# Kernel tuning notes

Measured on AMD Instinct MI355X. Metric: run time of the kernel, lower is better.

Reference implementation:

```python
import jax, jax.numpy as jnp
import numpy as np

N_NODES = 40000
N_EDGES = 640000
IN_F = 128
HID = 128
MAX_ITERS = 8  # torch loop runs MAX_ITERS + 1 state updates (epsilon=None)


def setup_inputs() -> dict:
    key = jax.random.key(0)
    k1, k2, k3, k4, k5, k6 = jax.random.split(key, 6)
    x = jax.random.normal(k1, (N_NODES, IN_F), dtype=jnp.float32)
    edge_index = jax.random.randint(k2, (2, N_EDGES), 0, N_NODES, dtype=jnp.int64)
    scale = 0.1 / np.sqrt(HID)  # keep tanh out of deep saturation (ESN-style spectral scaling)
    w_in0 = jax.random.normal(k3, (HID, IN_F), dtype=jnp.float32) * scale   # layer 0 input_weight
    w_rec0 = jax.random.normal(k4, (HID, HID), dtype=jnp.float32) * scale   # layer 0 recurrent_weight
    w_in1 = jax.random.normal(k5, (HID, HID), dtype=jnp.float32) * scale    # layer 1 input_weight
    w_rec1 = jax.random.normal(k6, (HID, HID), dtype=jnp.float32) * scale   # layer 1 recurrent_weight
    return {"edge_index": edge_index, "x": x,
            "w_in0": w_in0, "w_rec0": w_rec0, "w_in1": w_in1, "w_rec1": w_rec1}


def _embed(x_proj, w_rec, src, dst):
    # Fixed-point iteration: state = tanh(x_proj + aggr(state) @ w_rec)
    # aggr = sum of source-node states scattered to destination nodes (PyG aggr='add').
    state0 = jnp.zeros_like(x_proj)

    def step(state, _):
        aggr = jax.ops.segment_sum(state[src], dst, num_segments=N_NODES)  # [N, H]
        new_state = jnp.tanh(x_proj + aggr @ w_rec)
        return new_state, None

    state, _ = jax.lax.scan(step, state0, None, length=MAX_ITERS + 1)
    return state


def reference(edge_index, x, w_in0, w_rec0, w_in1, w_rec1):
    src, dst = edge_index[0], edge_index[1]
    h0 = _embed(x @ w_in0.T, w_rec0, src, dst)    # layer 0 embeddings [N, H]
    h1 = _embed(h0 @ w_in1.T, w_rec1, src, dst)   # layer 1 embeddings [N, H]
    return h1  # fully=False, pooling=None -> final layer node embeddings
```

## Files before the change

kernel.cpp:

```cpp
#include <hip/hip_runtime.h>
#include <math.h>

#define N_NODES 40000
#define N_EDGES 640000
#define HID 128
#define MAXW 64
#define ITERS 8
#define NH (N_NODES * HID)

typedef __bf16 bf16x8 __attribute__((ext_vector_type(8)));
typedef __bf16 bf16x4 __attribute__((ext_vector_type(4)));
typedef float floatx4 __attribute__((ext_vector_type(4)));

__global__ __launch_bounds__(256) void init_kernel(int* __restrict__ ell,
                                                   int* __restrict__ deg,
                                                   __bf16* __restrict__ padA,
                                                   __bf16* __restrict__ padB) {
    int i = blockIdx.x * 256 + threadIdx.x;
    int4 pad = {N_NODES, N_NODES, N_NODES, N_NODES};
    ((int4*)ell)[i] = pad;
    if (i < N_NODES) deg[i] = 0;
    if (i < HID / 8) {
        bf16x8 z;
#pragma unroll
        for (int j = 0; j < 8; ++j) z[j] = (__bf16)0.f;
        ((bf16x8*)padA)[i] = z;
        ((bf16x8*)padB)[i] = z;
    }
}

__global__ __launch_bounds__(256) void build_ell_kernel(const int* __restrict__ ei,
                                                        int* __restrict__ deg,
                                                        int* __restrict__ ell) {
    int e = blockIdx.x * 256 + threadIdx.x;
    if (e >= N_EDGES) return;
    int s = ei[e];
    int d = ei[N_EDGES + e];
    int c = atomicAdd(&deg[d], 1);
    if (c < MAXW) ell[d * MAXW + c] = s;
}

__global__ __launch_bounds__(256) void pack_w_kernel(const float* __restrict__ w,
                                                     __bf16* __restrict__ pk, int trans) {
    int f = blockIdx.x * 256 + threadIdx.x;
    int j = f & 7, l = (f >> 3) & 63, t = (f >> 9) & 7, c = f >> 12;
    int k = c * 32 + (l >> 4) * 8 + j;
    int n = t * 16 + (l & 15);
    float v = trans ? w[n * HID + k] : w[k * HID + n];
    pk[f] = (__bf16)v;
}

__global__ __launch_bounds__(256) void cast_bf16_kernel(const float* __restrict__ x,
                                                        __bf16* __restrict__ o) {
    int i = blockIdx.x * 256 + threadIdx.x;
    float4 v = ((const float4*)x)[i];
    bf16x4 b;
    b[0] = (__bf16)v.x; b[1] = (__bf16)v.y; b[2] = (__bf16)v.z; b[3] = (__bf16)v.w;
    ((bf16x4*)o)[i] = b;
}

__global__ __launch_bounds__(256) void mfma_gemm_kernel(const __bf16* A,
                                                        const __bf16* __restrict__ Bpk,
                                                        float* __restrict__ raw_out,
                                                        __bf16* st_bf) {
    __shared__ float tile[4][16][132];
    int tid = threadIdx.x;
    int wv = tid >> 6, lane = tid & 63;
    int q = lane >> 4, cl = lane & 15;

    int row_a = blockIdx.x * 64 + wv * 16 + cl;
    bf16x8 a[4];
#pragma unroll
    for (int c = 0; c < 4; ++c)
        a[c] = *(const bf16x8*)(A + (size_t)row_a * HID + c * 32 + q * 8);

#pragma unroll
    for (int t = 0; t < 8; ++t) {
        floatx4 acc_t = {0.f, 0.f, 0.f, 0.f};
#pragma unroll
        for (int c = 0; c < 4; ++c) {
            bf16x8 b = *(const bf16x8*)(Bpk + (((c * 8 + t) * 64 + lane) << 3));
            acc_t = __builtin_amdgcn_mfma_f32_16x16x32_bf16(a[c], b, acc_t, 0, 0, 0);
        }
#pragma unroll
        for (int r = 0; r < 4; ++r)
            tile[wv][q * 4 + r][t * 16 + cl] = acc_t[r];
    }
    int row = lane >> 2, seg = lane & 3;
    size_t goff = (size_t)(blockIdx.x * 64 + wv * 16 + row) * HID + seg * 32;
    float v[32];
#pragma unroll
    for (int j = 0; j < 8; ++j) {
        floatx4 t4 = *(floatx4*)&tile[wv][row][seg * 32 + j * 4];
        v[j * 4] = t4[0]; v[j * 4 + 1] = t4[1]; v[j * 4 + 2] = t4[2]; v[j * 4 + 3] = t4[3];
        float4 o = {t4[0], t4[1], t4[2], t4[3]};
        *(float4*)(raw_out + goff + j * 4) = o;
    }
#pragma unroll
    for (int i = 0; i < 32; ++i) v[i] = tanhf(v[i]);
#pragma unroll
    for (int j = 0; j < 4; ++j) {
        bf16x8 o;
#pragma unroll
        for (int k = 0; k < 8; ++k) o[k] = (__bf16)v[j * 8 + k];
        *(bf16x8*)(st_bf + goff + j * 8) = o;
    }
}

__global__ __launch_bounds__(256) void fused_iter_kernel(
    const __bf16* __restrict__ state_in,
    __bf16* __restrict__ state_out,
    const int* __restrict__ ell,
    const int* __restrict__ deg,
    const __bf16* __restrict__ Bpk,
    const float* __restrict__ xproj,
    float* __restrict__ st_f32) {
    __shared__ __align__(16) char smem[17408];
    int(*ell_lds)[68] = (int(*)[68])smem;
    __bf16(*aggr_lds)[136] = (__bf16(*)[136])(smem + 8704);
    float(*tile)[16][68] = (float(*)[16][68])smem;

    int tid = threadIdx.x;
    int wv = tid >> 6, lane = tid & 63;
    int q = lane >> 4, f = lane & 15;
    int nb = blockIdx.x * 32;

#pragma unroll
    for (int i = 0; i < 2; ++i) {
        int g = tid * 2 + i;
        int n = g >> 4, c = (g & 15) << 2;
        int4 v = *(const int4*)&ell[(nb + n) * MAXW + c];
        *(int4*)&ell_lds[n][c] = v;
    }
    int degv = deg[nb + (lane & 31)];
    __syncthreads();

    int n0 = wv * 8 + q;
    int n1 = wv * 8 + 4 + q;
    int cnt0 = __shfl(degv, n0); if (cnt0 > MAXW) cnt0 = MAXW;
    int cnt1 = __shfl(degv, n1); if (cnt1 > MAXW) cnt1 = MAXW;
    int ga = (cnt0 + 3) >> 2, gb = (cnt1 + 3) >> 2;
    int gmax = ga > gb ? ga : gb;
    float acc0[8], acc1[8];
#pragma unroll
    for (int j = 0; j < 8; ++j) { acc0[j] = 0.f; acc1[j] = 0.f; }
    for (int g = 0; g < gmax; ++g) {
        int base = g * 4;
        int sA0 = ell_lds[n0][base + 0];
        int sA1 = ell_lds[n0][base + 1];
        int sA2 = ell_lds[n0][base + 2];
        int sA3 = ell_lds[n0][base + 3];
        int sB0 = ell_lds[n1][base + 0];
        int sB1 = ell_lds[n1][base + 1];
        int sB2 = ell_lds[n1][base + 2];
        int sB3 = ell_lds[n1][base + 3];
        bf16x8 vA0 = *(const bf16x8*)(state_in + (size_t)sA0 * HID + f * 8);
        bf16x8 vA1 = *(const bf16x8*)(state_in + (size_t)sA1 * HID + f * 8);
        bf16x8 vA2 = *(const bf16x8*)(state_in + (size_t)sA2 * HID + f * 8);
        bf16x8 vA3 = *(const bf16x8*)(state_in + (size_t)sA3 * HID + f * 8);
        bf16x8 vB0 = *(const bf16x8*)(state_in + (size_t)sB0 * HID + f * 8);
        bf16x8 vB1 = *(const bf16x8*)(state_in + (size_t)sB1 * HID + f * 8);
        bf16x8 vB2 = *(const bf16x8*)(state_in + (size_t)sB2 * HID + f * 8);
        bf16x8 vB3 = *(const bf16x8*)(state_in + (size_t)sB3 * HID + f * 8);
#pragma unroll
        for (int j = 0; j < 8; ++j) {
            acc0[j] += ((float)vA0[j] + (float)vA1[j]) + ((float)vA2[j] + (float)vA3[j]);
            acc1[j] += ((float)vB0[j] + (float)vB1[j]) + ((float)vB2[j] + (float)vB3[j]);
        }
    }
    {
        bf16x8 o0, o1;
#pragma unroll
        for (int j = 0; j < 8; ++j) { o0[j] = (__bf16)acc0[j]; o1[j] = (__bf16)acc1[j]; }
        *(bf16x8*)&aggr_lds[n0][f * 8] = o0;
        *(bf16x8*)&aggr_lds[n1][f * 8] = o1;
    }
    __syncthreads();

    int rg = wv >> 1, h = wv & 1;
    bf16x8 a[4];
#pragma unroll
    for (int c = 0; c < 4; ++c)
        a[c] = *(const bf16x8*)&aggr_lds[rg * 16 + f][c * 32 + q * 8];
    __syncthreads();

#pragma unroll
    for (int t = 0; t < 4; ++t) {
        floatx4 acc_t = {0.f, 0.f, 0.f, 0.f};
#pragma unroll
        for (int c = 0; c < 4; ++c) {
            bf16x8 b = *(const bf16x8*)(Bpk + (((c * 8 + h * 4 + t) * 64 + lane) << 3));
            acc_t = __builtin_amdgcn_mfma_f32_16x16x32_bf16(a[c], b, acc_t, 0, 0, 0);
        }
#pragma unroll
        for (int r = 0; r < 4; ++r)
            tile[wv][q * 4 + r][t * 16 + f] = acc_t[r];
    }

    int row = lane >> 2, seg = lane & 3;
    size_t goff = (size_t)(nb + rg * 16 + row) * HID + h * 64 + seg * 16;
    float v[16];
#pragma unroll
    for (int j = 0; j < 4; ++j) {
        floatx4 t4 = *(floatx4*)&tile[wv][row][seg * 16 + j * 4];
        float4 b = *(const float4*)(xproj + goff + j * 4);
        v[j * 4] = t4[0] + b.x;
        v[j * 4 + 1] = t4[1] + b.y;
        v[j * 4 + 2] = t4[2] + b.z;
        v[j * 4 + 3] = t4[3] + b.w;
    }
#pragma unroll
    for (int i = 0; i < 16; ++i) v[i] = tanhf(v[i]);
#pragma unroll
    for (int j = 0; j < 2; ++j) {
        bf16x8 o;
#pragma unroll
        for (int k = 0; k < 8; ++k) o[k] = (__bf16)v[j * 8 + k];
        *(bf16x8*)(state_out + goff + j * 8) = o;
    }
    if (st_f32) {
#pragma unroll
        for (int j = 0; j < 4; ++j) {
            float4 o = {v[j * 4], v[j * 4 + 1], v[j * 4 + 2], v[j * 4 + 3]};
            *(float4*)(st_f32 + goff + j * 4) = o;
        }
    }
}

extern "C" void kernel_launch(void* const* d_in, const int* in_sizes, int n_in,
                              void* d_out, int out_size, void* d_ws, size_t ws_size,
                              hipStream_t stream) {
    const int* ei = (const int*)d_in[0];
    const float* x = (const float*)d_in[1];
    const float* w_in0 = (const float*)d_in[2];
    const float* w_rec0 = (const float*)d_in[3];
    const float* w_in1 = (const float*)d_in[4];
    const float* w_rec1 = (const float*)d_in[5];
    float* out = (float*)d_out;

    float* xproj = (float*)d_ws;
    __bf16* stateA = (__bf16*)(xproj + NH);
    __bf16* stateB = stateA + NH + HID;
    __bf16* packs = stateB + NH + HID;
    int* deg = (int*)(packs + 4 * 16384);
    int* ell = deg + N_NODES;
    __bf16* pk_in0 = packs;
    __bf16* pk_rec0 = packs + 16384;
    __bf16* pk_in1 = packs + 2 * 16384;
    __bf16* pk_rec1 = packs + 3 * 16384;

    init_kernel<<<N_EDGES / 256, 256, 0, stream>>>(ell, deg, stateA + NH, stateB + NH);
    build_ell_kernel<<<N_EDGES / 256, 256, 0, stream>>>(ei, deg, ell);
    pack_w_kernel<<<64, 256, 0, stream>>>(w_in0, pk_in0, 1);
    pack_w_kernel<<<64, 256, 0, stream>>>(w_rec0, pk_rec0, 0);
    pack_w_kernel<<<64, 256, 0, stream>>>(w_in1, pk_in1, 1);
    pack_w_kernel<<<64, 256, 0, stream>>>(w_rec1, pk_rec1, 0);
    cast_bf16_kernel<<<NH / 4 / 256, 256, 0, stream>>>(x, stateB);

    for (int layer = 0; layer < 2; ++layer) {
        const __bf16* pk_in = layer ? pk_in1 : pk_in0;
        const __bf16* pk_rec = layer ? pk_rec1 : pk_rec0;
        const __bf16* xin = layer ? stateA : stateB;
        mfma_gemm_kernel<<<625, 256, 0, stream>>>(xin, pk_in, xproj, stateA);
        for (int it = 0; it < ITERS; ++it) {
            const __bf16* sin = (it & 1) ? stateB : stateA;
            __bf16* sout = (it & 1) ? stateA : stateB;
            float* f32out = (layer == 1 && it == ITERS - 1) ? out : nullptr;
            fused_iter_kernel<<<N_NODES / 32, 256, 0, stream>>>(sin, sout, ell, deg,
                                                                pk_rec, xproj, f32out);
        }
    }
}
```

Before: 589.6 us.

## Store xproj in bf16, load only used ELL columns, unroll gather by 8

The input projection is now stored as bf16 instead of fp32, which halves the xproj traffic read by every iteration kernel. A per-block max-degree array is built with atomicMax during ELL construction, so each block copies only the ELL columns it actually uses into LDS. The neighbor gather loop now issues 8 loads per node per step instead of 4 to raise memory-level parallelism. In exchange, xproj loses precision, the ELL build gains extra atomics, and the loop pads edge counts to a multiple of 8.

```diff
diff --git a/kernel.cpp b/kernel.cpp
--- a/kernel.cpp
+++ b/kernel.cpp
@@ -7,6 +7,7 @@
 #define MAXW 64
 #define ITERS 8
 #define NH (N_NODES * HID)
+#define NBLK (N_NODES / 32)
 
 typedef __bf16 bf16x8 __attribute__((ext_vector_type(8)));
 typedef __bf16 bf16x4 __attribute__((ext_vector_type(4)));
@@ -14,12 +15,14 @@
 
 __global__ __launch_bounds__(256) void init_kernel(int* __restrict__ ell,
                                                    int* __restrict__ deg,
+                                                   int* __restrict__ bmax,
                                                    __bf16* __restrict__ padA,
                                                    __bf16* __restrict__ padB) {
     int i = blockIdx.x * 256 + threadIdx.x;
     int4 pad = {N_NODES, N_NODES, N_NODES, N_NODES};
     ((int4*)ell)[i] = pad;
     if (i < N_NODES) deg[i] = 0;
+    if (i < NBLK) bmax[i] = 0;
     if (i < HID / 8) {
         bf16x8 z;
 #pragma unroll
@@ -31,13 +34,17 @@
 
 __global__ __launch_bounds__(256) void build_ell_kernel(const int* __restrict__ ei,
                                                         int* __restrict__ deg,
+                                                        int* __restrict__ bmax,
                                                         int* __restrict__ ell) {
     int e = blockIdx.x * 256 + threadIdx.x;
     if (e >= N_EDGES) return;
     int s = ei[e];
     int d = ei[N_EDGES + e];
     int c = atomicAdd(&deg[d], 1);
-    if (c < MAXW) ell[d * MAXW + c] = s;
+    if (c < MAXW) {
+        ell[d * MAXW + c] = s;
+        atomicMax(&bmax[d >> 5], c + 1);
+    }
 }
 
 __global__ __launch_bounds__(256) void pack_w_kernel(const float* __restrict__ w,
@@ -61,7 +68,7 @@
 
 __global__ __launch_bounds__(256) void mfma_gemm_kernel(const __bf16* A,
                                                         const __bf16* __restrict__ Bpk,
-                                                        float* __restrict__ raw_out,
+                                                        __bf16* __restrict__ xp_bf,
                                                         __bf16* st_bf) {
     __shared__ float tile[4][16][132];
     int tid = threadIdx.x;
@@ -93,8 +100,13 @@
     for (int j = 0; j < 8; ++j) {
         floatx4 t4 = *(floatx4*)&tile[wv][row][seg * 32 + j * 4];
         v[j * 4] = t4[0]; v[j * 4 + 1] = t4[1]; v[j * 4 + 2] = t4[2]; v[j * 4 + 3] = t4[3];
-        float4 o = {t4[0], t4[1], t4[2], t4[3]};
-        *(float4*)(raw_out + goff + j * 4) = o;
+    }
+#pragma unroll
+    for (int j = 0; j < 4; ++j) {
+        bf16x8 o;
+#pragma unroll
+        for (int k = 0; k < 8; ++k) o[k] = (__bf16)v[j * 8 + k];
+        *(bf16x8*)(xp_bf + goff + j * 8) = o;
     }
 #pragma unroll
     for (int i = 0; i < 32; ++i) v[i] = tanhf(v[i]);
@@ -112,8 +124,9 @@
     __bf16* __restrict__ state_out,
     const int* __restrict__ ell,
     const int* __restrict__ deg,
+    const int* __restrict__ bmax,
     const __bf16* __restrict__ Bpk,
-    const float* __restrict__ xproj,
+    const __bf16* __restrict__ xproj,
     float* __restrict__ st_f32) {
     __shared__ __align__(16) char smem[17408];
     int(*ell_lds)[68] = (int(*)[68])smem;
@@ -125,47 +138,42 @@
     int q = lane >> 4, f = lane & 15;
     int nb = blockIdx.x * 32;
 
-#pragma unroll
-    for (int i = 0; i < 2; ++i) {
-        int g = tid * 2 + i;
-        int n = g >> 4, c = (g & 15) << 2;
-        int4 v = *(const int4*)&ell[(nb + n) * MAXW + c];
-        *(int4*)&ell_lds[n][c] = v;
+    int gcnt = ((bmax[blockIdx.x] + 7) >> 3) << 1;
+    for (int g = tid >> 5; g < gcnt; g += 8) {
+        int n = tid & 31;
+        *(int4*)&ell_lds[n][g * 4] = *(const int4*)&ell[(nb + n) * MAXW + g * 4];
     }
     int degv = deg[nb + (lane & 31)];
     __syncthreads();
 
     int n0 = wv * 8 + q;
     int n1 = wv * 8 + 4 + q;
-    int cnt0 = __shfl(degv, n0); if (cnt0 > MAXW) cnt0 = MAXW;
-    int cnt1 = __shfl(degv, n1); if (cnt1 > MAXW) cnt1 = MAXW;
-    int ga = (cnt0 + 3) >> 2, gb = (cnt1 + 3) >> 2;
-    int gmax = ga > gb ? ga : gb;
+    int c0 = __shfl(degv, n0), c1 = __shfl(degv, n1);
+    int cm = c0 > c1 ? c0 : c1;
+    if (cm > MAXW) cm = MAXW;
+    int gmax = ((cm + 7) >> 3) << 1;
     float acc0[8], acc1[8];
 #pragma unroll
     for (int j = 0; j < 8; ++j) { acc0[j] = 0.f; acc1[j] = 0.f; }
-    for (int g = 0; g < gmax; ++g) {
-        int base = g * 4;
-        int sA0 = ell_lds[n0][base + 0];
-        int sA1 = ell_lds[n0][base + 1];
-        int sA2 = ell_lds[n0][base + 2];
-        int sA3 = ell_lds[n0][base + 3];
-        int sB0 = ell_lds[n1][base + 0];
-        int sB1 = ell_lds[n1][base + 1];
-        int sB2 = ell_lds[n1][base + 2];
-        int sB3 = ell_lds[n1][base + 3];
-        bf16x8 vA0 = *(const bf16x8*)(state_in + (size_t)sA0 * HID + f * 8);
-        bf16x8 vA1 = *(const bf16x8*)(state_in + (size_t)sA1 * HID + f * 8);
-        bf16x8 vA2 = *(const bf16x8*)(state_in + (size_t)sA2 * HID + f * 8);
-        bf16x8 vA3 = *(const bf16x8*)(state_in + (size_t)sA3 * HID + f * 8);
-        bf16x8 vB0 = *(const bf16x8*)(state_in + (size_t)sB0 * HID + f * 8);
-        bf16x8 vB1 = *(const bf16x8*)(state_in + (size_t)sB1 * HID + f * 8);
-        bf16x8 vB2 = *(const bf16x8*)(state_in + (size_t)sB2 * HID + f * 8);
-        bf16x8 vB3 = *(const bf16x8*)(state_in + (size_t)sB3 * HID + f * 8);
+    for (int g = 0; g < gmax; g += 2) {
+        int b0 = g * 4;
+        int sA[8], sB[8];
+#pragma unroll
+        for (int u = 0; u < 8; ++u) { sA[u] = ell_lds[n0][b0 + u]; sB[u] = ell_lds[n1][b0 + u]; }
+        bf16x8 vA[8], vB[8];
+#pragma unroll
+        for (int u = 0; u < 8; ++u)
+            vA[u] = *(const bf16x8*)(state_in + (size_t)sA[u] * HID + f * 8);
+#pragma unroll
+        for (int u = 0; u < 8; ++u)
+            vB[u] = *(const bf16x8*)(state_in + (size_t)sB[u] * HID + f * 8);
 #pragma unroll
         for (int j = 0; j < 8; ++j) {
-            acc0[j] += ((float)vA0[j] + (float)vA1[j]) + ((float)vA2[j] + (float)vA3[j]);
-            acc1[j] += ((float)vB0[j] + (float)vB1[j]) + ((float)vB2[j] + (float)vB3[j]);
+            float a0 = 0.f, a1 = 0.f;
+#pragma unroll
+            for (int u = 0; u < 8; ++u) { a0 += (float)vA[u][j]; a1 += (float)vB[u][j]; }
+            acc0[j] += a0;
+            acc1[j] += a1;
         }
     }
     {
@@ -200,15 +208,15 @@
     int row = lane >> 2, seg = lane & 3;
     size_t goff = (size_t)(nb + rg * 16 + row) * HID + h * 64 + seg * 16;
     float v[16];
+    bf16x8 bx0 = *(const bf16x8*)(xproj + goff);
+    bf16x8 bx1 = *(const bf16x8*)(xproj + goff + 8);
 #pragma unroll
     for (int j = 0; j < 4; ++j) {
         floatx4 t4 = *(floatx4*)&tile[wv][row][seg * 16 + j * 4];
-        float4 b = *(const float4*)(xproj + goff + j * 4);
-        v[j * 4] = t4[0] + b.x;
-        v[j * 4 + 1] = t4[1] + b.y;
-        v[j * 4 + 2] = t4[2] + b.z;
-        v[j * 4 + 3] = t4[3] + b.w;
-    }
+        v[j * 4] = t4[0]; v[j * 4 + 1] = t4[1]; v[j * 4 + 2] = t4[2]; v[j * 4 + 3] = t4[3];
+    }
+#pragma unroll
+    for (int k = 0; k < 8; ++k) { v[k] += (float)bx0[k]; v[8 + k] += (float)bx1[k]; }
 #pragma unroll
     for (int i = 0; i < 16; ++i) v[i] = tanhf(v[i]);
 #pragma unroll
@@ -238,19 +246,21 @@
     const float* w_rec1 = (const float*)d_in[5];
     float* out = (float*)d_out;
 
-    float* xproj = (float*)d_ws;
-    __bf16* stateA = (__bf16*)(xproj + NH);
+    __bf16* xproj_bf = (__bf16*)d_ws;
+    __bf16* stateA = xproj_bf + NH;
     __bf16* stateB = stateA + NH + HID;
     __bf16* packs = stateB + NH + HID;
     int* deg = (int*)(packs + 4 * 16384);
-    int* ell = deg + N_NODES;
+    int* bmax = deg + N_NODES;
+    int* ell = bmax + NBLK;
     __bf16* pk_in0 = packs;
     __bf16* pk_rec0 = packs + 16384;
     __bf16* pk_in1 = packs + 2 * 16384;
     __bf16* pk_rec1 = packs + 3 * 16384;
 
-    init_kernel<<<N_EDGES / 256, 256, 0, stream>>>(ell, deg, stateA + NH, stateB + NH);
-    build_ell_kernel<<<N_EDGES / 256, 256, 0, stream>>>(ei, deg, ell);
+    init_kernel<<<N_EDGES / 256, 256, 0, stream>>>(ell, deg, bmax, stateA + NH,
+                                                   stateB + NH);
+    build_ell_kernel<<<N_EDGES / 256, 256, 0, stream>>>(ei, deg, bmax, ell);
     pack_w_kernel<<<64, 256, 0, stream>>>(w_in0, pk_in0, 1);
     pack_w_kernel<<<64, 256, 0, stream>>>(w_rec0, pk_rec0, 0);
     pack_w_kernel<<<64, 256, 0, stream>>>(w_in1, pk_in1, 1);
@@ -261,13 +271,13 @@
         const __bf16* pk_in = layer ? pk_in1 : pk_in0;
         const __bf16* pk_rec = layer ? pk_rec1 : pk_rec0;
         const __bf16* xin = layer ? stateA : stateB;
-        mfma_gemm_kernel<<<625, 256, 0, stream>>>(xin, pk_in, xproj, stateA);
+        mfma_gemm_kernel<<<625, 256, 0, stream>>>(xin, pk_in, xproj_bf, stateA);
         for (int it = 0; it < ITERS; ++it) {
             const __bf16* sin = (it & 1) ? stateB : stateA;
             __bf16* sout = (it & 1) ? stateA : stateB;
             float* f32out = (layer == 1 && it == ITERS - 1) ? out : nullptr;
-            fused_iter_kernel<<<N_NODES / 32, 256, 0, stream>>>(sin, sout, ell, deg,
-                                                                pk_rec, xproj, f32out);
-        }
-    }
-}
+            fused_iter_kernel<<<NBLK, 256, 0, stream>>>(sin, sout, ell, deg, bmax,
+                                                        pk_rec, xproj_bf, f32out);
+        }
+    }
+}
```

Result: slower. 740.4 us (+25.6%).
